# Optimization experiments

Measured on AMD Instinct MI355X. Metric: run time of the kernel, lower is better.

Reference implementation:

```python
import jax, jax.numpy as jnp
import numpy as np

IN_C = 256
CC = 256
K_HP = 3  # highpass_kernel
ENC_K = 3  # encoder_kernel, dilation 1 -> padding 1


def _conv2d(x, w, b, pad):
    # x: [n, ci, h, w], w: [co, ci, kh, kw] (OIHW), b: [co]
    y = jax.lax.conv_general_dilated(
        x, w, window_strides=(1, 1), padding=((pad, pad), (pad, pad)),
        dimension_numbers=("NCHW", "OIHW", "NCHW"))
    return y + b[None, :, None, None]


def _kernel_normalizer(mask, k, hamming_flat):
    # mask: [n, k*k, h, w] (mask_channel = 1, scale_factor = 1 -> pixel_shuffle is identity)
    n, kc, h, w = mask.shape
    m = jax.nn.softmax(mask, axis=1)              # softmax over the k*k kernel taps
    m = m * hamming_flat[None, :, None, None]     # per-tap hamming window (row-major kxk)
    m = m / jnp.sum(m, axis=1, keepdims=True)     # renormalize to sum 1 per pixel
    return m


def _carafe(x, mask, k):
    # Content-aware reassembly, scale=1, group=1.
    # out[n,c,h,w] = sum_{i,j} mask[n, i*k+j, h, w] * x[n, c, h+i-k//2, w+j-k//2]
    pad = k // 2
    n, c, h, w = x.shape
    xp = jnp.pad(x, ((0, 0), (0, 0), (pad, pad), (pad, pad)))
    out = jnp.zeros_like(x)
    for i in range(k):
        for j in range(k):
            out = out + mask[:, i * k + j][:, None] * xp[:, :, i:i + h, j:j + w]
    return out


def setup_inputs() -> dict:
    key = jax.random.key(0)
    ks = jax.random.split(key, 6)
    n, h, w = 4, 128, 128
    s = 0.02
    x = jax.random.normal(ks[0], (n, IN_C, h, w), jnp.float32)
    w_comp = jax.random.normal(ks[1], (CC, IN_C, 1, 1), jnp.float32) * s
    b_comp = jnp.zeros((CC,), jnp.float32)
    w_hp = jax.random.normal(ks[2], (K_HP * K_HP, CC, ENC_K, ENC_K), jnp.float32) * s
    b_hp = jnp.zeros((K_HP * K_HP,), jnp.float32)
    w_res = jax.random.normal(ks[3], (CC, CC, ENC_K, ENC_K), jnp.float32) * s
    b_res = jnp.zeros((CC,), jnp.float32)
    w_mul = jax.random.normal(ks[4], (CC, CC, ENC_K, ENC_K), jnp.float32) * s
    b_mul = jnp.zeros((CC,), jnp.float32)
    ham = np.outer(np.hamming(K_HP), np.hamming(K_HP)).astype(np.float32).reshape(-1)
    hamming_hp = jnp.asarray(ham)
    return {"x": x, "w_comp": w_comp, "b_comp": b_comp, "w_hp": w_hp, "b_hp": b_hp,
            "w_res": w_res, "b_res": b_res, "w_mul": w_mul, "b_mul": b_mul,
            "hamming_hp": hamming_hp}


def reference(x, w_comp, b_comp, w_hp, b_hp, w_res, b_res, w_mul, b_mul, hamming_hp):
    compressed = _conv2d(x, w_comp, b_comp, 0)
    # high-pass branch: dynamic-kernel generation + CARAFE reassembly
    filt = _conv2d(compressed, w_hp, b_hp, (ENC_K - 1) // 2)
    filt = _kernel_normalizer(filt, K_HP, hamming_hp)
    feat_hp = x - _carafe(x, filt, K_HP)
    # additive residual branch
    feat_add = x + _conv2d(compressed, w_res, b_res, (ENC_K - 1) // 2)
    # multiplicative gating branch
    feat_mul = x * _conv2d(compressed, w_mul, b_mul, (ENC_K - 1) // 2)
    return (feat_hp, feat_add, feat_mul)
```

## Files before the change

kernel.cpp:

```cpp
#include <hip/hip_runtime.h>
#include <hip/hip_bf16.h>

#define NIMG 4
#define C    256
#define H    128
#define W    128
#define HW   (H*W)
#define CHW  (C*HW)
#define TOT  (NIMG*CHW)

typedef short bf16x8 __attribute__((ext_vector_type(8)));
typedef float f32x16 __attribute__((ext_vector_type(16)));
typedef unsigned short u16;

__device__ inline u16 f2bf(float f) {
    __hip_bfloat16 h = __float2bfloat16(f);
    return __builtin_bit_cast(u16, h);
}

__global__ __launch_bounds__(256)
void prep_w_kernel(const float* __restrict__ w_hp, const float* __restrict__ w_res,
                   const float* __restrict__ w_mul, const float* __restrict__ w_comp,
                   u16* __restrict__ wcat, u16* __restrict__ wbf)
{
    int i = blockIdx.x * 256 + threadIdx.x;
    const int NW = 576 * 2304;
    if (i < NW) {
        int co = i / 2304, r = i - co * 2304;
        int tap = r >> 8, ci = r & 255;
        float v = 0.f;
        if (co < 9)        v = w_hp[co * 2304 + ci * 9 + tap];
        else if (co < 265) v = w_res[(co - 9) * 2304 + ci * 9 + tap];
        else if (co < 521) v = w_mul[(co - 265) * 2304 + ci * 9 + tap];
        wcat[i] = f2bf(v);
    } else if (i < NW + 65536) {
        int j = i - NW;
        wbf[j] = f2bf(w_comp[j]);
    }
}

__global__ __launch_bounds__(256)
void conv1x1_mfma_kernel(const float* __restrict__ x, const u16* __restrict__ wbf,
                         const float* __restrict__ b, u16* __restrict__ comp)
{
    __shared__ u16 As[64 * 40];
    __shared__ u16 Bs[256 * 40];

    const int pt  = blockIdx.x;
    const int n   = pt >> 6;
    const int hw0 = (pt & 63) * 256;
    const int co0 = blockIdx.y * 64;

    const int tid  = threadIdx.x;
    const int wv   = tid >> 6;
    const int lane = tid & 63;
    const int l31  = lane & 31;
    const int lh   = lane >> 5;

    f32x16 acc[2][2];
    #pragma unroll
    for (int cf = 0; cf < 2; ++cf)
        #pragma unroll
        for (int p = 0; p < 2; ++p)
            #pragma unroll
            for (int e = 0; e < 16; ++e) acc[cf][p][e] = 0.f;

    for (int c0 = 0; c0 < 256; c0 += 32) {
        #pragma unroll
        for (int r = 0; r < 2; ++r) {
            int l  = tid + 256*r;
            int co = l >> 3, cq = l & 7;
            ushort4 v = *(const ushort4*)(wbf + (co0+co)*256 + c0 + cq*4);
            *(ushort4*)(As + co*40 + cq*4) = v;
        }
        #pragma unroll
        for (int r = 0; r < 2; ++r) {
            int l = tid + 256*r;
            int q = l & 7, g = l >> 3;
            const float* src = x + (long)n*CHW + (long)(c0 + q*4)*HW + hw0 + g*4;
            float4 v0 = *(const float4*)(src);
            float4 v1 = *(const float4*)(src + HW);
            float4 v2 = *(const float4*)(src + 2*HW);
            float4 v3 = *(const float4*)(src + 3*HW);
            u16* dst = Bs + (g*4)*40 + q*4;
            *(ushort4*)(dst)       = make_ushort4(f2bf(v0.x), f2bf(v1.x), f2bf(v2.x), f2bf(v3.x));
            *(ushort4*)(dst + 40)  = make_ushort4(f2bf(v0.y), f2bf(v1.y), f2bf(v2.y), f2bf(v3.y));
            *(ushort4*)(dst + 80)  = make_ushort4(f2bf(v0.z), f2bf(v1.z), f2bf(v2.z), f2bf(v3.z));
            *(ushort4*)(dst + 120) = make_ushort4(f2bf(v0.w), f2bf(v1.w), f2bf(v2.w), f2bf(v3.w));
        }
        __syncthreads();
        #pragma unroll
        for (int kk = 0; kk < 2; ++kk) {
            bf16x8 a0 = *(const bf16x8*)(As + (l31     )*40 + kk*16 + lh*8);
            bf16x8 a1 = *(const bf16x8*)(As + (l31 + 32)*40 + kk*16 + lh*8);
            #pragma unroll
            for (int p = 0; p < 2; ++p) {
                bf16x8 bb = *(const bf16x8*)(Bs + (wv*64 + p*32 + l31)*40 + kk*16 + lh*8);
                acc[0][p] = __builtin_amdgcn_mfma_f32_32x32x16_bf16(a0, bb, acc[0][p], 0, 0, 0);
                acc[1][p] = __builtin_amdgcn_mfma_f32_32x32x16_bf16(a1, bb, acc[1][p], 0, 0, 0);
            }
        }
        __syncthreads();
    }

    #pragma unroll
    for (int cf = 0; cf < 2; ++cf) {
        #pragma unroll
        for (int p = 0; p < 2; ++p) {
            int pos = hw0 + wv*64 + p*32 + l31;
            #pragma unroll
            for (int reg = 0; reg < 16; ++reg) {
                int row = (reg & 3) + 8*(reg >> 2) + 4*lh;
                int co  = co0 + cf*32 + row;
                comp[(long)n*CHW + (long)co*HW + pos] = f2bf(acc[cf][p][reg] + b[co]);
            }
        }
    }
}

__global__ __launch_bounds__(256, 2)
void conv3x3_mfma_kernel(const u16* __restrict__ comp, const u16* __restrict__ wcat,
                         const float* __restrict__ xin,
                         const float* __restrict__ b_hp, const float* __restrict__ b_res,
                         const float* __restrict__ b_mul,
                         float* __restrict__ out, float* __restrict__ filt_raw)
{
    __shared__ u16 As[64 * 152];
    __shared__ u16 Bs[6 * 132 * 24];

    const int pt  = blockIdx.x;
    const int n   = pt >> 5;
    const int y0  = (pt & 31) * 4;
    const int co0 = blockIdx.y * 64;

    const int tid  = threadIdx.x;
    const int wv   = tid >> 6;
    const int lane = tid & 63;
    const int l31  = lane & 31;
    const int lh   = lane >> 5;

    for (int i = tid; i < 6*132*24/2; i += 256) ((int*)Bs)[i] = 0;

    f32x16 acc[2][4];
    #pragma unroll
    for (int cf = 0; cf < 2; ++cf)
        #pragma unroll
        for (int p = 0; p < 4; ++p)
            #pragma unroll
            for (int e = 0; e < 16; ++e) acc[cf][p][e] = 0.f;

    const u16* wbase = wcat + (long)co0 * 2304;

    const u16* asrc[9]; u16* adst[9];
    #pragma unroll
    for (int r = 0; r < 9; ++r) {
        int l  = tid + 256*r;
        int co = l / 36, u = l - co*36;
        int tap = u >> 2, ciq = u & 3;
        asrc[r] = wbase + co*2304 + tap*256 + ciq*4;
        adst[r] = As + co*152 + tap*16 + ciq*4;
    }
    const u16* bsrc[3]; u16* bdst[3]; bool bvld[3];
    #pragma unroll
    for (int rr = 0; rr < 3; ++rr) {
        int l = tid + 256*rr;
        int q = l & 3, t = l >> 2;
        int r = t >> 5, g = t & 31;
        int yy = y0 - 1 + r;
        bvld[rr] = (yy >= 0 && yy < H);
        int yc = bvld[rr] ? yy : 0;
        bsrc[rr] = comp + ((long)n*C + q*4)*HW + yc*W + g*4;
        bdst[rr] = Bs + (r*132 + g*4 + 1)*24 + q*4;
    }

    __syncthreads();

    ushort4 pb[3][4];
    #pragma unroll
    for (int rr = 0; rr < 3; ++rr)
        if (bvld[rr]) {
            const u16* s = bsrc[rr];
            pb[rr][0] = *(const ushort4*)(s);
            pb[rr][1] = *(const ushort4*)(s + HW);
            pb[rr][2] = *(const ushort4*)(s + 2*HW);
            pb[rr][3] = *(const ushort4*)(s + 3*HW);
        }

    for (int c = 0; c < 16; ++c) {
        const int c0 = c * 16;
        #pragma unroll
        for (int r = 0; r < 9; ++r) {
            ushort4 v = *(const ushort4*)(asrc[r] + c0);
            *(ushort4*)(adst[r]) = v;
        }
        #pragma unroll
        for (int rr = 0; rr < 3; ++rr)
            if (bvld[rr]) {
                u16* d = bdst[rr];
                *(ushort4*)(d)      = make_ushort4(pb[rr][0].x, pb[rr][1].x, pb[rr][2].x, pb[rr][3].x);
                *(ushort4*)(d + 24) = make_ushort4(pb[rr][0].y, pb[rr][1].y, pb[rr][2].y, pb[rr][3].y);
                *(ushort4*)(d + 48) = make_ushort4(pb[rr][0].z, pb[rr][1].z, pb[rr][2].z, pb[rr][3].z);
                *(ushort4*)(d + 72) = make_ushort4(pb[rr][0].w, pb[rr][1].w, pb[rr][2].w, pb[rr][3].w);
            }
        __syncthreads();
        if (c < 15) {
            const long koff = (long)(c0 + 16) * HW;
            #pragma unroll
            for (int rr = 0; rr < 3; ++rr)
                if (bvld[rr]) {
                    const u16* s = bsrc[rr] + koff;
                    pb[rr][0] = *(const ushort4*)(s);
                    pb[rr][1] = *(const ushort4*)(s + HW);
                    pb[rr][2] = *(const ushort4*)(s + 2*HW);
                    pb[rr][3] = *(const ushort4*)(s + 3*HW);
                }
        }
        #pragma unroll
        for (int tap = 0; tap < 9; ++tap) {
            const int kh = tap / 3, kw = tap - kh*3;
            bf16x8 a0 = *(const bf16x8*)(As + (l31      )*152 + tap*16 + lh*8);
            bf16x8 a1 = *(const bf16x8*)(As + (l31 + 32 )*152 + tap*16 + lh*8);
            #pragma unroll
            for (int p = 0; p < 4; ++p) {
                bf16x8 bfr = *(const bf16x8*)(Bs + ((wv+kh)*132 + p*32 + l31 + kw)*24 + lh*8);
                acc[0][p] = __builtin_amdgcn_mfma_f32_32x32x16_bf16(a0, bfr, acc[0][p], 0, 0, 0);
                acc[1][p] = __builtin_amdgcn_mfma_f32_32x32x16_bf16(a1, bfr, acc[1][p], 0, 0, 0);
            }
        }
        __syncthreads();
    }

    const int yrow = y0 + wv;
    #pragma unroll
    for (int cf = 0; cf < 2; ++cf) {
        #pragma unroll
        for (int p = 0; p < 4; ++p) {
            #pragma unroll
            for (int reg = 0; reg < 16; ++reg) {
                int row = (reg & 3) + 8*(reg >> 2) + 4*lh;
                int co  = co0 + cf*32 + row;
                int xx  = p*32 + l31;
                float v = acc[cf][p][reg];
                if (co < 9) {
                    filt_raw[((long)n*9 + co)*HW + yrow*W + xx] = v + b_hp[co];
                } else if (co < 265) {
                    int c = co - 9;
                    long idx = (long)n*CHW + (long)c*HW + yrow*W + xx;
                    out[(long)TOT + idx] = xin[idx] + v + b_res[c];
                } else if (co < 521) {
                    int c = co - 265;
                    long idx = (long)n*CHW + (long)c*HW + yrow*W + xx;
                    out[2L*TOT + idx] = xin[idx] * (v + b_mul[c]);
                }
            }
        }
    }
}

__global__ __launch_bounds__(256)
void carafe_hp_kernel(const float* __restrict__ x, const float* __restrict__ filt_raw,
                      const float* __restrict__ ham, float* __restrict__ out)
{
    const int pt = blockIdx.x;
    const int n  = pt >> 7;
    const int y  = pt & 127;
    const int pg = threadIdx.x & 31;
    const int cs = threadIdx.x >> 5;
    const int x0 = pg * 4;

    float4 wt[9];
    {
        const float* fr = filt_raw + (long)n*9*HW + y*W + x0;
        #pragma unroll
        for (int t = 0; t < 9; ++t) wt[t] = *(const float4*)(fr + t*HW);
        float4 mx = wt[0];
        #pragma unroll
        for (int t = 1; t < 9; ++t) {
            mx.x = fmaxf(mx.x, wt[t].x); mx.y = fmaxf(mx.y, wt[t].y);
            mx.z = fmaxf(mx.z, wt[t].z); mx.w = fmaxf(mx.w, wt[t].w);
        }
        float4 s = make_float4(0,0,0,0);
        #pragma unroll
        for (int t = 0; t < 9; ++t) {
            float hm = ham[t];
            wt[t].x = expf(wt[t].x - mx.x) * hm; s.x += wt[t].x;
            wt[t].y = expf(wt[t].y - mx.y) * hm; s.y += wt[t].y;
            wt[t].z = expf(wt[t].z - mx.z) * hm; s.z += wt[t].z;
            wt[t].w = expf(wt[t].w - mx.w) * hm; s.w += wt[t].w;
        }
        float4 inv = make_float4(1.f/s.x, 1.f/s.y, 1.f/s.z, 1.f/s.w);
        #pragma unroll
        for (int t = 0; t < 9; ++t) {
            wt[t].x *= inv.x; wt[t].y *= inv.y; wt[t].z *= inv.z; wt[t].w *= inv.w;
        }
    }

    const float* xb = x   + (long)n*CHW + (long)y*W + x0;
    float*       ob = out + (long)n*CHW + (long)y*W + x0;

    for (int i = 0; i < 32; ++i) {
        int c = cs*32 + i;
        const float* xc = xb + (long)c*HW;
        float rr[3][6];
        #pragma unroll
        for (int dh = 0; dh < 3; ++dh) {
            int yy = y - 1 + dh;
            if (yy >= 0 && yy < H) {
                const float* p = xc + (dh-1)*W;
                float4 v = *(const float4*)p;
                rr[dh][0] = (x0 > 0)     ? p[-1] : 0.f;
                rr[dh][1] = v.x; rr[dh][2] = v.y; rr[dh][3] = v.z; rr[dh][4] = v.w;
                rr[dh][5] = (x0 + 4 < W) ? p[4]  : 0.f;
            } else {
                #pragma unroll
                for (int j = 0; j < 6; ++j) rr[dh][j] = 0.f;
            }
        }
        float4 a = make_float4(0,0,0,0);
        #pragma unroll
        for (int dh = 0; dh < 3; ++dh)
            #pragma unroll
            for (int kw = 0; kw < 3; ++kw) {
                float4 wv = wt[dh*3+kw];
                a.x += wv.x * rr[dh][kw];
                a.y += wv.y * rr[dh][kw+1];
                a.z += wv.z * rr[dh][kw+2];
                a.w += wv.w * rr[dh][kw+3];
            }
        float4 o;
        o.x = rr[1][1] - a.x; o.y = rr[1][2] - a.y;
        o.z = rr[1][3] - a.z; o.w = rr[1][4] - a.w;
        *(float4*)(ob + (long)c*HW) = o;
    }
}

extern "C" void kernel_launch(void* const* d_in, const int* in_sizes, int n_in,
                              void* d_out, int out_size, void* d_ws, size_t ws_size,
                              hipStream_t stream)
{
    const float* x      = (const float*)d_in[0];
    const float* w_comp = (const float*)d_in[1];
    const float* b_comp = (const float*)d_in[2];
    const float* w_hp   = (const float*)d_in[3];
    const float* b_hp   = (const float*)d_in[4];
    const float* w_res  = (const float*)d_in[5];
    const float* b_res  = (const float*)d_in[6];
    const float* w_mul  = (const float*)d_in[7];
    const float* b_mul  = (const float*)d_in[8];
    const float* ham    = (const float*)d_in[9];
    float* out = (float*)d_out;

    u16*   comp = (u16*)d_ws;
    float* filt = (float*)((char*)d_ws + (size_t)TOT*2);
    u16*   wcat = (u16*)((char*)d_ws + (size_t)TOT*2 + 2359296);
    u16*   wbf  = (u16*)((char*)d_ws + (size_t)TOT*2 + 2359296 + 2654208);

    const int NW = 576*2304;
    prep_w_kernel<<<(NW + 65536 + 255)/256, 256, 0, stream>>>(w_hp, w_res, w_mul, w_comp, wcat, wbf);
    conv1x1_mfma_kernel<<<dim3(256, 4), 256, 0, stream>>>(x, wbf, b_comp, comp);
    conv3x3_mfma_kernel<<<dim3(NIMG*H/4, 9), 256, 0, stream>>>(
        comp, wcat, x, b_hp, b_res, b_mul, out, filt);
    carafe_hp_kernel<<<NIMG*H, 256, 0, stream>>>(x, filt, ham, out);
}
```

Before: 375.6 us.

## Double-buffer weight tile via direct global-to-LDS loads with swizzled layout

Replaces the register-staged weight copy in the 3x3 conv MFMA kernel with global_load_lds 16-byte direct-to-LDS transfers into a double-buffered, XOR-swizzled A tile. The next chunk's weights are issued before computing the current chunk, and the B tile prefetch is pipelined one further stage using manual vmcnt/lgkmcnt waits and raw s_barrier. The aim is to hide global-load latency and cut register and instruction overhead in the main loop. The hand-counted waitcnt values are fragile and depend on the number of valid halo rows.

```diff
diff --git a/kernel.cpp b/kernel.cpp
--- a/kernel.cpp
+++ b/kernel.cpp
@@ -16,6 +16,12 @@
 __device__ inline u16 f2bf(float f) {
     __hip_bfloat16 h = __float2bfloat16(f);
     return __builtin_bit_cast(u16, h);
+}
+
+__device__ __forceinline__ void gld_lds16(const u16* g, u16* l) {
+    __builtin_amdgcn_global_load_lds(
+        (const __attribute__((address_space(1))) void*)g,
+        (__attribute__((address_space(3))) void*)l, 16, 0, 0);
 }
 
 __global__ __launch_bounds__(256)
@@ -125,7 +131,7 @@
                          const float* __restrict__ b_mul,
                          float* __restrict__ out, float* __restrict__ filt_raw)
 {
-    __shared__ u16 As[64 * 152];
+    __shared__ u16 As[2 * 64 * 144];
     __shared__ u16 Bs[6 * 132 * 24];
 
     const int pt  = blockIdx.x;
@@ -149,17 +155,25 @@
             #pragma unroll
             for (int e = 0; e < 16; ++e) acc[cf][p][e] = 0.f;
 
-    const u16* wbase = wcat + (long)co0 * 2304;
-
-    const u16* asrc[9]; u16* adst[9];
-    #pragma unroll
-    for (int r = 0; r < 9; ++r) {
-        int l  = tid + 256*r;
-        int co = l / 36, u = l - co*36;
-        int tap = u >> 2, ciq = u & 3;
-        asrc[r] = wbase + co*2304 + tap*256 + ciq*4;
-        adst[r] = As + co*152 + tap*16 + ciq*4;
-    }
+    const u16* wtile = wcat + (long)co0 * 2304;
+
+    const int nA = (wv < 2) ? 5 : 4;
+    int aoffs[5];
+    #pragma unroll
+    for (int r = 0; r < 5; ++r) {
+        int t = wv + 4*r;
+        aoffs[r] = 0;
+        if (t < 18) {
+            int item = t*64 + lane;
+            int row  = item / 18;
+            int j0   = item - row*18;
+            int j    = j0 ^ ((row >> 2) & 1);
+            aoffs[r] = row*2304 + (j >> 1)*256 + (j & 1)*8;
+        }
+    }
+    const int aoff0 = ((l31     )*288 + lh*16) ^ ((l31 & 4) << 2);
+    const int aoff1 = ((l31 + 32)*288 + lh*16) ^ ((l31 & 4) << 2);
+
     const u16* bsrc[3]; u16* bdst[3]; bool bvld[3];
     #pragma unroll
     for (int rr = 0; rr < 3; ++rr) {
@@ -172,6 +186,7 @@
         bsrc[rr] = comp + ((long)n*C + q*4)*HW + yc*W + g*4;
         bdst[rr] = Bs + (r*132 + g*4 + 1)*24 + q*4;
     }
+    const int nBv = (int)bvld[0] + (int)bvld[1] + (int)bvld[2];
 
     __syncthreads();
 
@@ -185,41 +200,52 @@
             pb[rr][2] = *(const ushort4*)(s + 2*HW);
             pb[rr][3] = *(const ushort4*)(s + 3*HW);
         }
+    #pragma unroll
+    for (int r = 0; r < 5; ++r)
+        if (r < nA) gld_lds16(wtile + aoffs[r], As + (wv + 4*r)*512);
+
+    asm volatile("s_waitcnt vmcnt(4)" ::: "memory");
+    __builtin_amdgcn_sched_barrier(0);
+    #pragma unroll
+    for (int rr = 0; rr < 3; ++rr)
+        if (bvld[rr]) {
+            u16* d = bdst[rr];
+            *(ushort4*)(d)      = make_ushort4(pb[rr][0].x, pb[rr][1].x, pb[rr][2].x, pb[rr][3].x);
+            *(ushort4*)(d + 24) = make_ushort4(pb[rr][0].y, pb[rr][1].y, pb[rr][2].y, pb[rr][3].y);
+            *(ushort4*)(d + 48) = make_ushort4(pb[rr][0].z, pb[rr][1].z, pb[rr][2].z, pb[rr][3].z);
+            *(ushort4*)(d + 72) = make_ushort4(pb[rr][0].w, pb[rr][1].w, pb[rr][2].w, pb[rr][3].w);
+        }
+    __builtin_amdgcn_sched_barrier(0);
+    #pragma unroll
+    for (int rr = 0; rr < 3; ++rr)
+        if (bvld[rr]) {
+            const u16* s = bsrc[rr] + (long)16*HW;
+            pb[rr][0] = *(const ushort4*)(s);
+            pb[rr][1] = *(const ushort4*)(s + HW);
+            pb[rr][2] = *(const ushort4*)(s + 2*HW);
+            pb[rr][3] = *(const ushort4*)(s + 3*HW);
+        }
+    asm volatile("s_waitcnt lgkmcnt(0)" ::: "memory");
+    if (nBv == 3) asm volatile("s_waitcnt vmcnt(12)" ::: "memory");
+    else          asm volatile("s_waitcnt vmcnt(8)"  ::: "memory");
+    __builtin_amdgcn_s_barrier();
+    __builtin_amdgcn_sched_barrier(0);
 
     for (int c = 0; c < 16; ++c) {
-        const int c0 = c * 16;
-        #pragma unroll
-        for (int r = 0; r < 9; ++r) {
-            ushort4 v = *(const ushort4*)(asrc[r] + c0);
-            *(ushort4*)(adst[r]) = v;
-        }
-        #pragma unroll
-        for (int rr = 0; rr < 3; ++rr)
-            if (bvld[rr]) {
-                u16* d = bdst[rr];
-                *(ushort4*)(d)      = make_ushort4(pb[rr][0].x, pb[rr][1].x, pb[rr][2].x, pb[rr][3].x);
-                *(ushort4*)(d + 24) = make_ushort4(pb[rr][0].y, pb[rr][1].y, pb[rr][2].y, pb[rr][3].y);
-                *(ushort4*)(d + 48) = make_ushort4(pb[rr][0].z, pb[rr][1].z, pb[rr][2].z, pb[rr][3].z);
-                *(ushort4*)(d + 72) = make_ushort4(pb[rr][0].w, pb[rr][1].w, pb[rr][2].w, pb[rr][3].w);
-            }
-        __syncthreads();
+        const int bsel = c & 1;
         if (c < 15) {
-            const long koff = (long)(c0 + 16) * HW;
-            #pragma unroll
-            for (int rr = 0; rr < 3; ++rr)
-                if (bvld[rr]) {
-                    const u16* s = bsrc[rr] + koff;
-                    pb[rr][0] = *(const ushort4*)(s);
-                    pb[rr][1] = *(const ushort4*)(s + HW);
-                    pb[rr][2] = *(const ushort4*)(s + 2*HW);
-                    pb[rr][3] = *(const ushort4*)(s + 3*HW);
-                }
-        }
+            const int c0n = (c + 1) * 16;
+            #pragma unroll
+            for (int r = 0; r < 5; ++r)
+                if (r < nA) gld_lds16(wtile + aoffs[r] + c0n,
+                                      As + (bsel^1)*9216 + (wv + 4*r)*512);
+        }
+        const char* Ab = (const char*)As + bsel*18432;
         #pragma unroll
         for (int tap = 0; tap < 9; ++tap) {
             const int kh = tap / 3, kw = tap - kh*3;
-            bf16x8 a0 = *(const bf16x8*)(As + (l31      )*152 + tap*16 + lh*8);
-            bf16x8 a1 = *(const bf16x8*)(As + (l31 + 32 )*152 + tap*16 + lh*8);
+            bf16x8 a0 = *(const bf16x8*)(Ab + (aoff0 + tap*32));
+            bf16x8 a1 = *(const bf16x8*)(Ab + (aoff1 + tap*32));
             #pragma unroll
             for (int p = 0; p < 4; ++p) {
                 bf16x8 bfr = *(const bf16x8*)(Bs + ((wv+kh)*132 + p*32 + l31 + kw)*24 + lh*8);
@@ -227,7 +253,40 @@
                 acc[1][p] = __builtin_amdgcn_mfma_f32_32x32x16_bf16(a1, bfr, acc[1][p], 0, 0, 0);
             }
         }
-        __syncthreads();
+        if (c < 15) {
+            __builtin_amdgcn_s_barrier();
+            __builtin_amdgcn_sched_barrier(0);
+            asm volatile("s_waitcnt vmcnt(4)" ::: "memory");
+            __builtin_amdgcn_sched_barrier(0);
+            #pragma unroll
+            for (int rr = 0; rr < 3; ++rr)
+                if (bvld[rr]) {
+                    u16* d = bdst[rr];
+                    *(ushort4*)(d)      = make_ushort4(pb[rr][0].x, pb[rr][1].x, pb[rr][2].x, pb[rr][3].x);
+                    *(ushort4*)(d + 24) = make_ushort4(pb[rr][0].y, pb[rr][1].y, pb[rr][2].y, pb[rr][3].y);
+                    *(ushort4*)(d + 48) = make_ushort4(pb[rr][0].z, pb[rr][1].z, pb[rr][2].z, pb[rr][3].z);
+                    *(ushort4*)(d + 72) = make_ushort4(pb[rr][0].w, pb[rr][1].w, pb[rr][2].w, pb[rr][3].w);
+                }
+            __builtin_amdgcn_sched_barrier(0);
+            if (c < 14) {
+                const long koff = (long)(c + 2) * 16 * HW;
+                #pragma unroll
+                for (int rr = 0; rr < 3; ++rr)
+                    if (bvld[rr]) {
+                        const u16* s = bsrc[rr] + koff;
+                        pb[rr][0] = *(const ushort4*)(s);
+                        pb[rr][1] = *(const ushort4*)(s + HW);
+                        pb[rr][2] = *(const ushort4*)(s + 2*HW);
+                        pb[rr][3] = *(const ushort4*)(s + 3*HW);
+                    }
+            }
+            asm volatile("s_waitcnt lgkmcnt(0)" ::: "memory");
+            if (c == 14)      asm volatile("s_waitcnt vmcnt(0)"  ::: "memory");
+            else if (nBv == 3) asm volatile("s_waitcnt vmcnt(12)" ::: "memory");
+            else              asm volatile("s_waitcnt vmcnt(8)"  ::: "memory");
+            __builtin_amdgcn_s_barrier();
+            __builtin_amdgcn_sched_barrier(0);
+        }
     }
 
     const int yrow = y0 + wv;
```

After: 389.4 us. 3.7% more time.

## Shrink 3x3 conv tile to two rows, swizzle LDS B tile, raise occupancy

Applied to the files above, without the earlier changes.

The 3x3 implicit-GEMM conv now gives each block two output rows instead of four. The four waves are split over 2 rows x 2 column halves, which halves accumulator registers per wave. The B tile in LDS drops its 24-element padding for a 16-element stride with an XOR swizzle to avoid bank conflicts, and A/B staging uses 8-wide vector loads and stores. Launch bounds move to 3 blocks per SM for higher occupancy. In exchange, halo rows are re-fetched more often (4 input rows per 2 output rows instead of 6 per 4), and there are twice as many blocks each reloading the weight tile.

```diff
diff --git a/kernel.cpp b/kernel.cpp
--- a/kernel.cpp
+++ b/kernel.cpp
@@ -10,12 +10,17 @@
 #define TOT  (NIMG*CHW)
 
 typedef short bf16x8 __attribute__((ext_vector_type(8)));
+typedef unsigned short ushort8 __attribute__((ext_vector_type(8)));
 typedef float f32x16 __attribute__((ext_vector_type(16)));
 typedef unsigned short u16;
 
 __device__ inline u16 f2bf(float f) {
     __hip_bfloat16 h = __float2bfloat16(f);
     return __builtin_bit_cast(u16, h);
+}
+
+__device__ __forceinline__ int swzB(int byte) {
+    return byte ^ (((byte >> 7) & 1) << 4) ^ (((byte >> 8) & 3) << 5);
 }
 
 __global__ __launch_bounds__(256)
@@ -118,7 +123,7 @@
     }
 }
 
-__global__ __launch_bounds__(256, 2)
+__global__ __launch_bounds__(256, 3)
 void conv3x3_mfma_kernel(const u16* __restrict__ comp, const u16* __restrict__ wcat,
                          const float* __restrict__ xin,
                          const float* __restrict__ b_hp, const float* __restrict__ b_res,
@@ -126,11 +131,11 @@
                          float* __restrict__ out, float* __restrict__ filt_raw)
 {
     __shared__ u16 As[64 * 152];
-    __shared__ u16 Bs[6 * 132 * 24];
+    __shared__ u16 Bs[4 * 132 * 16];
 
     const int pt  = blockIdx.x;
-    const int n   = pt >> 5;
-    const int y0  = (pt & 31) * 4;
+    const int n   = pt >> 6;
+    const int y0  = (pt & 63) * 2;
     const int co0 = blockIdx.y * 64;
 
     const int tid  = threadIdx.x;
@@ -138,119 +143,107 @@
     const int lane = tid & 63;
     const int l31  = lane & 31;
     const int lh   = lane >> 5;
-
-    for (int i = tid; i < 6*132*24/2; i += 256) ((int*)Bs)[i] = 0;
-
-    f32x16 acc[2][4];
+    const int row  = wv & 1;
+    const int ch   = wv >> 1;
+
+    for (int i = tid; i < 4*132*16/2; i += 256) ((int*)Bs)[i] = 0;
+
+    f32x16 acc[2][2];
     #pragma unroll
     for (int cf = 0; cf < 2; ++cf)
         #pragma unroll
-        for (int p = 0; p < 4; ++p)
+        for (int p = 0; p < 2; ++p)
             #pragma unroll
             for (int e = 0; e < 16; ++e) acc[cf][p][e] = 0.f;
 
     const u16* wbase = wcat + (long)co0 * 2304;
 
-    const u16* asrc[9]; u16* adst[9];
-    #pragma unroll
-    for (int r = 0; r < 9; ++r) {
-        int l  = tid + 256*r;
-        int co = l / 36, u = l - co*36;
-        int tap = u >> 2, ciq = u & 3;
-        asrc[r] = wbase + co*2304 + tap*256 + ciq*4;
-        adst[r] = As + co*152 + tap*16 + ciq*4;
-    }
-    const u16* bsrc[3]; u16* bdst[3]; bool bvld[3];
-    #pragma unroll
-    for (int rr = 0; rr < 3; ++rr) {
-        int l = tid + 256*rr;
-        int q = l & 3, t = l >> 2;
-        int r = t >> 5, g = t & 31;
-        int yy = y0 - 1 + r;
-        bvld[rr] = (yy >= 0 && yy < H);
-        int yc = bvld[rr] ? yy : 0;
-        bsrc[rr] = comp + ((long)n*C + q*4)*HW + yc*W + g*4;
-        bdst[rr] = Bs + (r*132 + g*4 + 1)*24 + q*4;
-    }
+    const u16* asrc[5]; u16* adst[5]; bool avld[5];
+    #pragma unroll
+    for (int r = 0; r < 5; ++r) {
+        int l = tid + 256*r;
+        avld[r] = (l < 1152);
+        int ll = avld[r] ? l : 0;
+        int co = ll / 18, s = ll - co*18;
+        asrc[r] = wbase + co*2304 + (s >> 1)*256 + (s & 1)*8;
+        adst[r] = As + co*152 + s*8;
+    }
+
+    const int bh  = lh;
+    const int bcg = l31;
+    const int byy = y0 - 1 + wv;
+    const bool bv = (byy >= 0 && byy < H);
+    const u16* bsrc = comp + ((long)n*C + bh*8)*HW + (bv ? byy : 0)*W + bcg*4;
 
     __syncthreads();
 
-    ushort4 pb[3][4];
-    #pragma unroll
-    for (int rr = 0; rr < 3; ++rr)
-        if (bvld[rr]) {
-            const u16* s = bsrc[rr];
-            pb[rr][0] = *(const ushort4*)(s);
-            pb[rr][1] = *(const ushort4*)(s + HW);
-            pb[rr][2] = *(const ushort4*)(s + 2*HW);
-            pb[rr][3] = *(const ushort4*)(s + 3*HW);
-        }
+    ushort4 pb[8];
+    if (bv) {
+        #pragma unroll
+        for (int j = 0; j < 8; ++j) pb[j] = *(const ushort4*)(bsrc + (long)j*HW);
+    }
 
     for (int c = 0; c < 16; ++c) {
         const int c0 = c * 16;
         #pragma unroll
-        for (int r = 0; r < 9; ++r) {
-            ushort4 v = *(const ushort4*)(asrc[r] + c0);
-            *(ushort4*)(adst[r]) = v;
-        }
-        #pragma unroll
-        for (int rr = 0; rr < 3; ++rr)
-            if (bvld[rr]) {
-                u16* d = bdst[rr];
-                *(ushort4*)(d)      = make_ushort4(pb[rr][0].x, pb[rr][1].x, pb[rr][2].x, pb[rr][3].x);
-                *(ushort4*)(d + 24) = make_ushort4(pb[rr][0].y, pb[rr][1].y, pb[rr][2].y, pb[rr][3].y);
-                *(ushort4*)(d + 48) = make_ushort4(pb[rr][0].z, pb[rr][1].z, pb[rr][2].z, pb[rr][3].z);
-                *(ushort4*)(d + 72) = make_ushort4(pb[rr][0].w, pb[rr][1].w, pb[rr][2].w, pb[rr][3].w);
-            }
+        for (int r = 0; r < 5; ++r)
+            if (avld[r]) {
+                ushort8 v = *(const ushort8*)(asrc[r] + c0);
+                *(ushort8*)(adst[r]) = v;
+            }
+        if (bv) {
+            #pragma unroll
+            for (int cw = 0; cw < 4; ++cw) {
+                ushort8 v;
+                #pragma unroll
+                for (int j = 0; j < 8; ++j) v[j] = ((const u16*)&pb[j])[cw];
+                int byteoff = ((wv*132 + bcg*4 + 1 + cw) << 5) + (bh << 4);
+                *(ushort8*)((char*)Bs + swzB(byteoff)) = v;
+            }
+        }
         __syncthreads();
-        if (c < 15) {
-            const long koff = (long)(c0 + 16) * HW;
-            #pragma unroll
-            for (int rr = 0; rr < 3; ++rr)
-                if (bvld[rr]) {
-                    const u16* s = bsrc[rr] + koff;
-                    pb[rr][0] = *(const ushort4*)(s);
-                    pb[rr][1] = *(const ushort4*)(s + HW);
-                    pb[rr][2] = *(const ushort4*)(s + 2*HW);
-                    pb[rr][3] = *(const ushort4*)(s + 3*HW);
-                }
+        if (c < 15 && bv) {
+            const u16* s = bsrc + (long)(c0 + 16)*HW;
+            #pragma unroll
+            for (int j = 0; j < 8; ++j) pb[j] = *(const ushort4*)(s + (long)j*HW);
         }
         #pragma unroll
         for (int tap = 0; tap < 9; ++tap) {
             const int kh = tap / 3, kw = tap - kh*3;
-            bf16x8 a0 = *(const bf16x8*)(As + (l31      )*152 + tap*16 + lh*8);
-            bf16x8 a1 = *(const bf16x8*)(As + (l31 + 32 )*152 + tap*16 + lh*8);
-            #pragma unroll
-            for (int p = 0; p < 4; ++p) {
-                bf16x8 bfr = *(const bf16x8*)(Bs + ((wv+kh)*132 + p*32 + l31 + kw)*24 + lh*8);
-                acc[0][p] = __builtin_amdgcn_mfma_f32_32x32x16_bf16(a0, bfr, acc[0][p], 0, 0, 0);
-                acc[1][p] = __builtin_amdgcn_mfma_f32_32x32x16_bf16(a1, bfr, acc[1][p], 0, 0, 0);
+            bf16x8 a0 = *(const bf16x8*)((const char*)As + l31*304      + tap*32 + lh*16);
+            bf16x8 a1 = *(const bf16x8*)((const char*)As + (l31+32)*304 + tap*32 + lh*16);
+            #pragma unroll
+            for (int p = 0; p < 2; ++p) {
+                int byteoff = (((row + kh)*132 + ch*64 + p*32 + l31 + kw) << 5) + (lh << 4);
+                bf16x8 bb = *(const bf16x8*)((const char*)Bs + swzB(byteoff));
+                acc[0][p] = __builtin_amdgcn_mfma_f32_32x32x16_bf16(a0, bb, acc[0][p], 0, 0, 0);
+                acc[1][p] = __builtin_amdgcn_mfma_f32_32x32x16_bf16(a1, bb, acc[1][p], 0, 0, 0);
             }
         }
         __syncthreads();
     }
 
-    const int yrow = y0 + wv;
+    const int yrow = y0 + row;
     #pragma unroll
     for (int cf = 0; cf < 2; ++cf) {
         #pragma unroll
-        for (int p = 0; p < 4; ++p) {
+        for (int p = 0; p < 2; ++p) {
+            int xx = ch*64 + p*32 + l31;
             #pragma unroll
             for (int reg = 0; reg < 16; ++reg) {
-                int row = (reg & 3) + 8*(reg >> 2) + 4*lh;
-                int co  = co0 + cf*32 + row;
-                int xx  = p*32 + l31;
+                int rw = (reg & 3) + 8*(reg >> 2) + 4*lh;
+                int co = co0 + cf*32 + rw;
                 float v = acc[cf][p][reg];
                 if (co < 9) {
                     filt_raw[((long)n*9 + co)*HW + yrow*W + xx] = v + b_hp[co];
                 } else if (co < 265) {
-                    int c = co - 9;
-                    long idx = (long)n*CHW + (long)c*HW + yrow*W + xx;
-                    out[(long)TOT + idx] = xin[idx] + v + b_res[c];
+                    int cc = co - 9;
+                    long idx = (long)n*CHW + (long)cc*HW + yrow*W + xx;
+                    out[(long)TOT + idx] = xin[idx] + v + b_res[cc];
                 } else if (co < 521) {
-                    int c = co - 265;
-                    long idx = (long)n*CHW + (long)c*HW + yrow*W + xx;
-                    out[2L*TOT + idx] = xin[idx] * (v + b_mul[c]);
+                    int cc = co - 265;
+                    long idx = (long)n*CHW + (long)cc*HW + yrow*W + xx;
+                    out[2L*TOT + idx] = xin[idx] * (v + b_mul[cc]);
                 }
             }
         }
@@ -358,7 +351,7 @@
     const int NW = 576*2304;
     prep_w_kernel<<<(NW + 65536 + 255)/256, 256, 0, stream>>>(w_hp, w_res, w_mul, w_comp, wcat, wbf);
     conv1x1_mfma_kernel<<<dim3(256, 4), 256, 0, stream>>>(x, wbf, b_comp, comp);
-    conv3x3_mfma_kernel<<<dim3(NIMG*H/4, 9), 256, 0, stream>>>(
+    conv3x3_mfma_kernel<<<dim3(NIMG*H/2, 9), 256, 0, stream>>>(
         comp, wcat, x, b_hp, b_res, b_mul, out, filt);
     carafe_hp_kernel<<<NIMG*H, 256, 0, stream>>>(x, filt, ham, out);
 }
```

Result: faster. 334.8 us (-10.9%).
